# Performance work log

Measured on AMD Instinct MI355X. Metric: run time of the kernel, lower is better.

The kernel has to match this reference:

```python
import jax, jax.numpy as jnp
import numpy as np

H = 128
IN = 5
EPS = 1e-5


def lstm(x, Wih, Whh, bih, bhh):
    # x: [B,T,D]; PyTorch gate order i,f,g,o along 4H axis
    B, T, _ = x.shape
    xW = jnp.einsum('btd,gd->btg', x, Wih) + bih + bhh  # [B,T,4H]
    WhhT = Whh.T

    def step(carry, xt):
        h, c = carry
        g = xt + h @ WhhT
        i, f, gg, o = jnp.split(g, 4, axis=-1)
        i = jax.nn.sigmoid(i)
        f = jax.nn.sigmoid(f)
        gg = jnp.tanh(gg)
        o = jax.nn.sigmoid(o)
        c = f * c + i * gg
        h = o * jnp.tanh(c)
        return (h, c), h

    h0 = jnp.zeros((B, H), x.dtype)
    _, hs = jax.lax.scan(step, (h0, h0), jnp.swapaxes(xW, 0, 1))
    return jnp.swapaxes(hs, 0, 1)  # [B,T,H]


def batchnorm(x, gamma, beta):
    # training-mode BN over (batch, time) per channel; x: [B,T,H]
    mean = jnp.mean(x, axis=(0, 1))
    var = jnp.var(x, axis=(0, 1))
    return (x - mean) * (gamma * jax.lax.rsqrt(var + EPS)) + beta


def forward_one(x, Wih1, Whh1, bih1, bhh1, g1, b1, Wih2, Whh2, bih2, bhh2, g2, b2, fcW, fcb):
    out = lstm(x, Wih1, Whh1, bih1, bhh1)
    out = batchnorm(out, g1, b1)
    # dropout is identity (eval / deterministic reference)
    out = lstm(out, Wih2, Whh2, bih2, bhh2)
    out = batchnorm(out, g2, b2)
    emb = out[:, -1, :] @ fcW.T + fcb  # [B,128]
    norm = jnp.sqrt(jnp.sum(emb * emb, axis=1, keepdims=True))
    return emb / jnp.maximum(norm, 1e-12)  # F.normalize p=2


def setup_inputs() -> dict:
    key = jax.random.key(0)
    ks = jax.random.split(key, 20)
    B, T = 512, 128
    s_in = 1.0 / np.sqrt(H)
    d = {
        'a': jax.random.normal(ks[0], (B, T, IN), jnp.float32),
        'p': jax.random.normal(ks[1], (B, T, IN), jnp.float32),
        'n': jax.random.normal(ks[2], (B, T, IN), jnp.float32),
        'Wih1': jax.random.uniform(ks[3], (4 * H, IN), jnp.float32, -s_in, s_in),
        'Whh1': jax.random.uniform(ks[4], (4 * H, H), jnp.float32, -s_in, s_in),
        'bih1': jax.random.uniform(ks[5], (4 * H,), jnp.float32, -s_in, s_in),
        'bhh1': jax.random.uniform(ks[6], (4 * H,), jnp.float32, -s_in, s_in),
        'g1': jnp.ones((H,), jnp.float32),
        'b1': jnp.zeros((H,), jnp.float32),
        'Wih2': jax.random.uniform(ks[7], (4 * H, H), jnp.float32, -s_in, s_in),
        'Whh2': jax.random.uniform(ks[8], (4 * H, H), jnp.float32, -s_in, s_in),
        'bih2': jax.random.uniform(ks[9], (4 * H,), jnp.float32, -s_in, s_in),
        'bhh2': jax.random.uniform(ks[10], (4 * H,), jnp.float32, -s_in, s_in),
        'g2': jnp.ones((H,), jnp.float32),
        'b2': jnp.zeros((H,), jnp.float32),
        'fcW': jax.random.uniform(ks[11], (H, H), jnp.float32, -s_in, s_in),
        'fcb': jax.random.uniform(ks[12], (H,), jnp.float32, -s_in, s_in),
    }
    return d


def reference(a, p, n, Wih1, Whh1, bih1, bhh1, g1, b1, Wih2, Whh2, bih2, bhh2, g2, b2, fcW, fcb):
    f = lambda x: forward_one(x, Wih1, Whh1, bih1, bhh1, g1, b1, Wih2, Whh2, bih2, bhh2, g2, b2, fcW, fcb)
    return (f(a), f(p), f(n))
```

## Files before the change

kernel.cpp:

```cpp
#include <hip/hip_runtime.h>


typedef __attribute__((ext_vector_type(8))) _Float16 half8;
typedef __attribute__((ext_vector_type(4))) float f32x4;

#define TS 128
#define HID 128
#define NGATE 512
#define INV_N (1.0f/65536.0f)

#define BAR() asm volatile("s_waitcnt lgkmcnt(0)\n\ts_barrier" ::: "memory")

__device__ __forceinline__ float rcpf(float x) { return __builtin_amdgcn_rcpf(x); }
__device__ __forceinline__ float clamp20(float x) { return fminf(fmaxf(x, -20.0f), 20.0f); }

__device__ __forceinline__ _Float16 lstm_cell(float zi, float zf, float zg, float zo,
                                              float& c) {
  zg = clamp20(zg);
  float ei = __expf(-zi);
  float eg = __expf(-2.0f * zg);
  float ef = __expf(-zf);
  float fv = rcpf(1.0f + ef);
  float ig = (1.0f - eg) * rcpf((1.0f + ei) * (1.0f + eg));
  float cc = fv * c + ig;
  c = cc;
  float ccl = clamp20(cc);
  float eo = __expf(-zo);
  float ec = __expf(-2.0f * ccl);
  float hv = (1.0f - ec) * rcpf((1.0f + eo) * (1.0f + ec));
  return (_Float16)hv;
}


__global__ void prep_all(const float* __restrict__ xa, const float* __restrict__ xp,
                         const float* __restrict__ xn,
                         const float* __restrict__ Whh1, const float* __restrict__ Whh2,
                         const float* __restrict__ bih1, const float* __restrict__ bhh1,
                         _Float16* __restrict__ xpad,
                         _Float16* __restrict__ whhT1, _Float16* __restrict__ whhT2,
                         float* __restrict__ b1c) {
  int bid = blockIdx.x, tid = threadIdx.x;
  if (bid < 6144) {
    int i = bid * 256 + tid;
    int tile = i >> 14, rem = i & 16383;
    int t = rem >> 7, r = (rem >> 3) & 15, d = i & 7;
    int inp = tile >> 5, rloc = (tile & 31) * 16;
    const float* x = (inp == 0) ? xa : ((inp == 1) ? xp : xn);
    xpad[i] = (d < 5) ? (_Float16)x[(rloc + r) * 640 + t * 5 + d] : (_Float16)0.0f;
  } else if (bid < 6656) {
    int i = (bid - 6144) * 256 + tid;
    int which = i >> 16, idx = i & 65535;
    int k = idx >> 9, g = idx & 511;
    const float* src = which ? Whh2 : Whh1;
    (which ? whhT2 : whhT1)[idx] = (_Float16)src[g * HID + k];
  } else {
    int i = (bid - 6656) * 256 + tid;
    b1c[i] = bih1[i] + bhh1[i];
  }
}

__global__ __launch_bounds__(512, 2) void lstm1_kernel(
    const _Float16* __restrict__ xpad,
    const float* __restrict__ Wih1,
    const float* __restrict__ b1c,
    const _Float16* __restrict__ whhT,
    _Float16* __restrict__ hs1,
    float* __restrict__ s1sum, float* __restrict__ s1sq) {
  const int wg = blockIdx.x;
  const int inp = wg >> 5;
  const int tid = threadIdx.x;
  const int w = tid >> 6;
  const int lane = tid & 63;
  const int l15 = lane & 15;
  const int quad = lane >> 4;
  const int col = w * 16 + l15;
  const int kb = quad * 8;

  __shared__ _Float16 hb[2][2048];
  for (int i = tid; i < 4096; i += 512) ((_Float16*)hb)[i] = (_Float16)0.0f;

  const int rbase = (quad * 16 + l15) * 8;
  const int wbase = (w >> 1) * 512 + ((w & 1) * 2 + (l15 >> 3)) * 128 +
                    quad * 32 + (l15 & 7);

  half8 bh[4][4];
#pragma unroll
  for (int kt = 0; kt < 4; ++kt)
#pragma unroll
    for (int gt = 0; gt < 4; ++gt) {
      int gcol = gt * 128 + col;
      half8 v;
#pragma unroll
      for (int j = 0; j < 8; ++j) v[j] = whhT[(kt * 32 + kb + j) * NGATE + gcol];
      bh[kt][gt] = v;
    }
  half8 bx[4];
#pragma unroll
  for (int gt = 0; gt < 4; ++gt) {
    half8 v = {0, 0, 0, 0, 0, 0, 0, 0};
    if (quad == 0) {
#pragma unroll
      for (int j = 0; j < 5; ++j) v[j] = (_Float16)Wih1[(gt * 128 + col) * 5 + j];
    }
    bx[gt] = v;
  }
  f32x4 biasv[4];
#pragma unroll
  for (int gt = 0; gt < 4; ++gt) {
    float b = b1c[gt * 128 + col];
    biasv[gt][0] = b; biasv[gt][1] = b; biasv[gt][2] = b; biasv[gt][3] = b;
  }

  half8 xp = {0, 0, 0, 0, 0, 0, 0, 0};
  if (quad == 0) xp = *(const half8*)&xpad[((size_t)(wg * TS) * 16 + l15) * 8];

  float c[4] = {0, 0, 0, 0};
  float ssum = 0.0f, ssq = 0.0f;
  _Float16* hs1w = hs1 + (size_t)wg * TS * 2048;

  __syncthreads();

  for (int t = 0; t < TS; ++t) {
    f32x4 acc[4];
#pragma unroll
    for (int gt = 0; gt < 4; ++gt)
      acc[gt] = __builtin_amdgcn_mfma_f32_16x16x32_f16(xp, bx[gt], biasv[gt], 0, 0, 0);
    if (t + 1 < TS && quad == 0)
      xp = *(const half8*)&xpad[((size_t)(wg * TS + t + 1) * 16 + l15) * 8];
    BAR();
    if (t > 0) {
      float2 cp = *(const float2*)&hb[t & 1][tid * 4];
      *(float2*)&hs1w[(size_t)(t - 1) * 2048 + tid * 4] = cp;
    }
#pragma unroll
    for (int kt = 0; kt < 4; ++kt) {
      half8 ah = *(const half8*)&hb[t & 1][kt * 512 + rbase];
#pragma unroll
      for (int gt = 0; gt < 4; ++gt)
        acc[gt] = __builtin_amdgcn_mfma_f32_16x16x32_f16(ah, bh[kt][gt], acc[gt], 0, 0, 0);
    }
    const int wb = (t + 1) & 1;
#pragma unroll
    for (int r = 0; r < 4; ++r) {
      _Float16 hh = lstm_cell(acc[0][r], acc[1][r], acc[2][r], acc[3][r], c[r]);
      float hr = (float)hh;
      ssum += hr; ssq += hr * hr;
      hb[wb][wbase + r * 8] = hh;
    }
  }
  BAR();
  {
    float2 cp = *(const float2*)&hb[0][tid * 4];
    *(float2*)&hs1w[(size_t)(TS - 1) * 2048 + tid * 4] = cp;
  }
  float s = ssum, q = ssq;
  s += __shfl_xor(s, 16); s += __shfl_xor(s, 32);
  q += __shfl_xor(q, 16); q += __shfl_xor(q, 32);
  if (quad == 0) {
    atomicAdd(&s1sum[inp * HID + col], s);
    atomicAdd(&s1sq[inp * HID + col], q);
  }
}

__global__ void mid_kernel(const float* __restrict__ s1sum, const float* __restrict__ s1sq,
                           const float* __restrict__ g1, const float* __restrict__ b1,
                           const float* __restrict__ Wih2,
                           const float* __restrict__ bih2, const float* __restrict__ bhh2,
                           _Float16* __restrict__ w2s, float* __restrict__ bias2eff) {
  int bid = blockIdx.x, tid = threadIdx.x;
  if (bid < 768) {
    int i = bid * 256 + tid;
    int inp = i >> 16, rem = i & 65535, k = rem >> 9, g = rem & 511;
    float m = s1sum[inp * HID + k] * INV_N;
    float v = s1sq[inp * HID + k] * INV_N - m * m;
    float sc = g1[k] * rsqrtf(v + 1e-5f);
    w2s[i] = (_Float16)(sc * Wih2[g * HID + k]);
  } else {
    int i = (bid - 768) * 256 + tid;
    int inp = i >> 9, g = i & 511;
    float acc = bih2[g] + bhh2[g];
    for (int h = 0; h < HID; ++h) {
      float m = s1sum[inp * HID + h] * INV_N;
      float v = s1sq[inp * HID + h] * INV_N - m * m;
      float sc = g1[h] * rsqrtf(v + 1e-5f);
      acc += (b1[h] - m * sc) * Wih2[g * HID + h];
    }
    bias2eff[i] = acc;
  }
}

__global__ __launch_bounds__(512, 2) void lstm2_kernel(
    const _Float16* __restrict__ hs1,
    const _Float16* __restrict__ whhT2,
    const _Float16* __restrict__ w2s,
    const float* __restrict__ bias2eff,
    _Float16* __restrict__ h_last,
    float* __restrict__ s2sum, float* __restrict__ s2sq) {
  const int wg = blockIdx.x;
  const int inp = wg >> 5;
  const int gr0 = wg * 16;
  const int tid = threadIdx.x;
  const int w = tid >> 6;
  const int lane = tid & 63;
  const int l15 = lane & 15;
  const int quad = lane >> 4;
  const int col = w * 16 + l15;
  const int kb = quad * 8;

  __shared__ _Float16 hb[2][2048];
  for (int i = tid; i < 4096; i += 512) ((_Float16*)hb)[i] = (_Float16)0.0f;

  const int rbase = (quad * 16 + l15) * 8;
  const int wbase = (w >> 1) * 512 + ((w & 1) * 2 + (l15 >> 3)) * 128 +
                    quad * 32 + (l15 & 7);

  const _Float16* w2sI = w2s + (size_t)inp * HID * NGATE;
  half8 bh[4][4], bxw[4][4];
#pragma unroll
  for (int kt = 0; kt < 4; ++kt)
#pragma unroll
    for (int gt = 0; gt < 4; ++gt) {
      int gcol = gt * 128 + col;
      half8 vh, vx;
#pragma unroll
      for (int j = 0; j < 8; ++j) {
        vh[j] = whhT2[(kt * 32 + kb + j) * NGATE + gcol];
        vx[j] = w2sI[(kt * 32 + kb + j) * NGATE + gcol];
      }
      bh[kt][gt] = vh;
      bxw[kt][gt] = vx;
    }
  f32x4 biasv[4];
#pragma unroll
  for (int gt = 0; gt < 4; ++gt) {
    float b = bias2eff[inp * NGATE + gt * 128 + col];
    biasv[gt][0] = b; biasv[gt][1] = b; biasv[gt][2] = b; biasv[gt][3] = b;
  }

  const _Float16* hg = hs1 + (size_t)wg * TS * 2048;
  half8 a2A[4], a2B[4];
#pragma unroll
  for (int kt = 0; kt < 4; ++kt) {
    a2A[kt] = *(const half8*)&hg[kt * 512 + rbase];
    a2B[kt] = *(const half8*)&hg[(size_t)2048 + kt * 512 + rbase];
  }

  float c[4] = {0, 0, 0, 0};
  float ssum = 0.0f, ssq = 0.0f;

  __syncthreads();

  auto step = [&](int t, half8 (&cur)[4]) {
    f32x4 acc[4];
#pragma unroll
    for (int gt = 0; gt < 4; ++gt)
      acc[gt] = __builtin_amdgcn_mfma_f32_16x16x32_f16(cur[0], bxw[0][gt], biasv[gt], 0, 0, 0);
#pragma unroll
    for (int kt = 1; kt < 4; ++kt)
#pragma unroll
      for (int gt = 0; gt < 4; ++gt)
        acc[gt] = __builtin_amdgcn_mfma_f32_16x16x32_f16(cur[kt], bxw[kt][gt], acc[gt], 0, 0, 0);
    if (t + 2 < TS) {
#pragma unroll
      for (int kt = 0; kt < 4; ++kt)
        cur[kt] = *(const half8*)&hg[(size_t)(t + 2) * 2048 + kt * 512 + rbase];
    }
    BAR();
#pragma unroll
    for (int kt = 0; kt < 4; ++kt) {
      half8 ah = *(const half8*)&hb[t & 1][kt * 512 + rbase];
#pragma unroll
      for (int gt = 0; gt < 4; ++gt)
        acc[gt] = __builtin_amdgcn_mfma_f32_16x16x32_f16(ah, bh[kt][gt], acc[gt], 0, 0, 0);
    }
    const int wb = (t + 1) & 1;
#pragma unroll
    for (int r = 0; r < 4; ++r) {
      _Float16 hh = lstm_cell(acc[0][r], acc[1][r], acc[2][r], acc[3][r], c[r]);
      float hr = (float)hh;
      ssum += hr; ssq += hr * hr;
      hb[wb][wbase + r * 8] = hh;
      if (t == TS - 1) h_last[(size_t)(gr0 + quad * 4 + r) * HID + col] = hh;
    }
  };

  for (int t = 0; t < TS; t += 2) {
    step(t, a2A);
    step(t + 1, a2B);
  }

  float s = ssum, q = ssq;
  s += __shfl_xor(s, 16); s += __shfl_xor(s, 32);
  q += __shfl_xor(q, 16); q += __shfl_xor(q, 32);
  if (quad == 0) {
    atomicAdd(&s2sum[inp * HID + col], s);
    atomicAdd(&s2sq[inp * HID + col], q);
  }
}

__global__ __launch_bounds__(256, 1) void head_kernel(
    const _Float16* __restrict__ h_last,
    const float* __restrict__ s2sum, const float* __restrict__ s2sq,
    const float* __restrict__ g2, const float* __restrict__ b2,
    const float* __restrict__ fcW, const float* __restrict__ fcb,
    float* __restrict__ out) {
  const int wg = blockIdx.x;
  const int inp = wg >> 5;
  const int gr0 = wg * 16;
  const int tid = threadIdx.x;

  __shared__ float fcwT[128][132];
  __shared__ float bnh[16][132];
  __shared__ float s2[128], sh2[128];
  __shared__ float part[16][16];
  __shared__ float inv[16];

  if (tid < 128) {
    float m = s2sum[inp * HID + tid] * INV_N;
    float v = s2sq[inp * HID + tid] * INV_N - m * m;
    float s = g2[tid] * rsqrtf(v + 1e-5f);
    s2[tid] = s; sh2[tid] = b2[tid] - m * s;
  }
  for (int i = tid; i < 16384; i += 256) {
    int j = i >> 7, h = i & 127;
    fcwT[h][j] = fcW[i];
  }
  __syncthreads();
  {
    int row = tid >> 4, c0 = (tid & 15) * 8;
#pragma unroll
    for (int k = 0; k < 8; ++k) {
      int h = c0 + k;
      bnh[row][h] = (float)h_last[(gr0 + row) * HID + h] * s2[h] + sh2[h];
    }
  }
  __syncthreads();
  const int row = tid >> 4, jl = tid & 15;
  float emb[8];
  float sq = 0.0f;
#pragma unroll
  for (int jj = 0; jj < 8; ++jj) {
    int j = jl + jj * 16;
    float acc = fcb[j];
    for (int h = 0; h < HID; ++h) acc += bnh[row][h] * fcwT[h][j];
    emb[jj] = acc; sq += acc * acc;
  }
  part[row][jl] = sq;
  __syncthreads();
  if (tid < 16) {
    float s = 0.0f;
    for (int k = 0; k < 16; ++k) s += part[tid][k];
    float nrm = sqrtf(s);
    inv[tid] = 1.0f / fmaxf(nrm, 1e-12f);
  }
  __syncthreads();
#pragma unroll
  for (int jj = 0; jj < 8; ++jj)
    out[(gr0 + row) * HID + jl + jj * 16] = emb[jj] * inv[row];
}

extern "C" void kernel_launch(void* const* d_in, const int* in_sizes, int n_in,
                              void* d_out, int out_size, void* d_ws, size_t ws_size,
                              hipStream_t stream) {
  const float* a    = (const float*)d_in[0];
  const float* p    = (const float*)d_in[1];
  const float* nn   = (const float*)d_in[2];
  const float* Wih1 = (const float*)d_in[3];
  const float* Whh1 = (const float*)d_in[4];
  const float* bih1 = (const float*)d_in[5];
  const float* bhh1 = (const float*)d_in[6];
  const float* g1   = (const float*)d_in[7];
  const float* b1   = (const float*)d_in[8];
  const float* Wih2 = (const float*)d_in[9];
  const float* Whh2 = (const float*)d_in[10];
  const float* bih2 = (const float*)d_in[11];
  const float* bhh2 = (const float*)d_in[12];
  const float* g2   = (const float*)d_in[13];
  const float* b2   = (const float*)d_in[14];
  const float* fcW  = (const float*)d_in[15];
  const float* fcb  = (const float*)d_in[16];

  char* ws = (char*)d_ws;
  float* s1sum = (float*)(ws + 0);
  float* s1sq  = s1sum + 384;
  float* s2sum = s1sum + 768;
  float* s2sq  = s1sum + 1152;
  float* b1c      = (float*)(ws + 6144);
  float* bias2eff = (float*)(ws + 8192);
  _Float16* whhT1 = (_Float16*)(ws + 14336);
  _Float16* whhT2 = (_Float16*)(ws + 145408);
  _Float16* w2s   = (_Float16*)(ws + 276480);
  _Float16* hlast = (_Float16*)(ws + 669696);
  _Float16* xpad  = (_Float16*)(ws + 1062912);
  _Float16* hs1   = (_Float16*)(ws + 4208640);

  hipMemsetAsync(ws, 0, 6144, stream);

  prep_all<<<6658, 256, 0, stream>>>(a, p, nn, Whh1, Whh2, bih1, bhh1,
                                     xpad, whhT1, whhT2, b1c);
  lstm1_kernel<<<96, 512, 0, stream>>>(xpad, Wih1, b1c, whhT1, hs1, s1sum, s1sq);
  mid_kernel<<<774, 256, 0, stream>>>(s1sum, s1sq, g1, b1, Wih2, bih2, bhh2,
                                      w2s, bias2eff);
  lstm2_kernel<<<96, 512, 0, stream>>>(hs1, whhT2, w2s, bias2eff, hlast, s2sum, s2sq);
  head_kernel<<<96, 256, 0, stream>>>(hlast, s2sum, s2sq, g2, b2, fcW, fcb, (float*)d_out);
}
```

Measured before the change: 368.0 us.

## Fold exp2 scaling into weights, vectorize prep layouts, reorder recurrent step barriers

Pre-scales the gate weights and biases by -log2(e), or -2·log2(e) for the g gate, so the LSTM cell can use raw exp2 without multiplies, and clamps with fmed3. Weight layouts are changed so the recurrent kernels load half8 vectors directly instead of gathering scalars. The prep and mid kernels write 8 halves per thread and share BN scales through LDS, which cuts their grid sizes. In both recurrent loops the barrier moves to the top of each step with the LDS reads hoisted ahead of the MFMAs. BN statistics now come from fp32 h instead of the fp16-rounded value, and h_last is written once after the loop.

```diff
diff --git a/kernel.cpp b/kernel.cpp
--- a/kernel.cpp
+++ b/kernel.cpp
@@ -8,27 +8,33 @@
 #define HID 128
 #define NGATE 512
 #define INV_N (1.0f/65536.0f)
+#define NL2E  -1.4426950408889634f
+#define N2L2E -2.8853900817779268f
+#define GCLAMP 57.707801635558536f
 
 #define BAR() asm volatile("s_waitcnt lgkmcnt(0)\n\ts_barrier" ::: "memory")
 
 __device__ __forceinline__ float rcpf(float x) { return __builtin_amdgcn_rcpf(x); }
-__device__ __forceinline__ float clamp20(float x) { return fminf(fmaxf(x, -20.0f), 20.0f); }
-
-__device__ __forceinline__ _Float16 lstm_cell(float zi, float zf, float zg, float zo,
-                                              float& c) {
-  zg = clamp20(zg);
-  float ei = __expf(-zi);
-  float eg = __expf(-2.0f * zg);
-  float ef = __expf(-zf);
-  float fv = rcpf(1.0f + ef);
-  float ig = (1.0f - eg) * rcpf((1.0f + ei) * (1.0f + eg));
+__device__ __forceinline__ float ex2(float x) { return __builtin_amdgcn_exp2f(x); }
+
+__device__ __forceinline__ float lstm_cell(float zi, float zf, float zg, float zo,
+                                           float& c) {
+  float zgc = __builtin_amdgcn_fmed3f(zg, -GCLAMP, GCLAMP);
+  float ei = ex2(zi);
+  float ef = ex2(zf);
+  float eg = ex2(zgc);
+  float eo = ex2(zo);
+  float pi = 1.0f + ei, pg = 1.0f + eg, pf = 1.0f + ef;
+  float P = pi * pg;
+  float rd = rcpf(P * pf);
+  float fv = P * rd;
+  float ig = (1.0f - eg) * (pf * rd);
   float cc = fv * c + ig;
   c = cc;
-  float ccl = clamp20(cc);
-  float eo = __expf(-zo);
-  float ec = __expf(-2.0f * ccl);
+  float t2 = __builtin_amdgcn_fmed3f(cc * N2L2E, -GCLAMP, GCLAMP);
+  float ec = ex2(t2);
   float hv = (1.0f - ec) * rcpf((1.0f + eo) * (1.0f + ec));
-  return (_Float16)hv;
+  return hv;
 }
 
 
@@ -40,22 +46,32 @@
                          _Float16* __restrict__ whhT1, _Float16* __restrict__ whhT2,
                          float* __restrict__ b1c) {
   int bid = blockIdx.x, tid = threadIdx.x;
-  if (bid < 6144) {
+  if (bid < 768) {
     int i = bid * 256 + tid;
-    int tile = i >> 14, rem = i & 16383;
-    int t = rem >> 7, r = (rem >> 3) & 15, d = i & 7;
+    int tile = i >> 11, rem = i & 2047;
+    int t = rem >> 4, r = rem & 15;
     int inp = tile >> 5, rloc = (tile & 31) * 16;
     const float* x = (inp == 0) ? xa : ((inp == 1) ? xp : xn);
-    xpad[i] = (d < 5) ? (_Float16)x[(rloc + r) * 640 + t * 5 + d] : (_Float16)0.0f;
-  } else if (bid < 6656) {
-    int i = (bid - 6144) * 256 + tid;
-    int which = i >> 16, idx = i & 65535;
-    int k = idx >> 9, g = idx & 511;
+    const float* row = x + (size_t)(rloc + r) * 640 + t * 5;
+    half8 v = {0, 0, 0, 0, 0, 0, 0, 0};
+#pragma unroll
+    for (int j = 0; j < 5; ++j) v[j] = (_Float16)row[j];
+    *(half8*)&xpad[(size_t)i * 8] = v;
+  } else if (bid < 832) {
+    int i = (bid - 768) * 256 + tid;
+    int which = i >> 13, i8 = i & 8191;
+    int kq = i8 >> 9, g = i8 & 511;
+    int k0 = (kq >> 2) * 32 + (kq & 3) * 8;
+    float gs = ((g >> 7) == 2) ? N2L2E : NL2E;
     const float* src = which ? Whh2 : Whh1;
-    (which ? whhT2 : whhT1)[idx] = (_Float16)src[g * HID + k];
+    half8 v;
+#pragma unroll
+    for (int j = 0; j < 8; ++j) v[j] = (_Float16)(src[(size_t)g * HID + k0 + j] * gs);
+    *(half8*)&(which ? whhT2 : whhT1)[(size_t)i8 * 8] = v;
   } else {
-    int i = (bid - 6656) * 256 + tid;
-    b1c[i] = bih1[i] + bhh1[i];
+    int i = (bid - 832) * 256 + tid;
+    float gs = ((i >> 7) == 2) ? N2L2E : NL2E;
+    b1c[i] = (bih1[i] + bhh1[i]) * gs;
   }
 }
 
@@ -74,7 +90,6 @@
   const int l15 = lane & 15;
   const int quad = lane >> 4;
   const int col = w * 16 + l15;
-  const int kb = quad * 8;
 
   __shared__ _Float16 hb[2][2048];
   for (int i = tid; i < 4096; i += 512) ((_Float16*)hb)[i] = (_Float16)0.0f;
@@ -87,20 +102,17 @@
 #pragma unroll
   for (int kt = 0; kt < 4; ++kt)
 #pragma unroll
-    for (int gt = 0; gt < 4; ++gt) {
-      int gcol = gt * 128 + col;
-      half8 v;
-#pragma unroll
-      for (int j = 0; j < 8; ++j) v[j] = whhT[(kt * 32 + kb + j) * NGATE + gcol];
-      bh[kt][gt] = v;
-    }
+    for (int gt = 0; gt < 4; ++gt)
+      bh[kt][gt] = *(const half8*)&whhT[(size_t)((kt * 4 + quad) * 512 + gt * 128 + col) * 8];
+
   half8 bx[4];
 #pragma unroll
   for (int gt = 0; gt < 4; ++gt) {
     half8 v = {0, 0, 0, 0, 0, 0, 0, 0};
     if (quad == 0) {
-#pragma unroll
-      for (int j = 0; j < 5; ++j) v[j] = (_Float16)Wih1[(gt * 128 + col) * 5 + j];
+      float gs = (gt == 2) ? N2L2E : NL2E;
+#pragma unroll
+      for (int j = 0; j < 5; ++j) v[j] = (_Float16)(Wih1[(gt * 128 + col) * 5 + j] * gs);
     }
     bx[gt] = v;
   }
@@ -118,35 +130,37 @@
   float ssum = 0.0f, ssq = 0.0f;
   _Float16* hs1w = hs1 + (size_t)wg * TS * 2048;
 
-  __syncthreads();
-
   for (int t = 0; t < TS; ++t) {
+    BAR();
+    half8 ah[4];
+#pragma unroll
+    for (int kt = 0; kt < 4; ++kt)
+      ah[kt] = *(const half8*)&hb[t & 1][kt * 512 + rbase];
+    if (t > 0) {
+      float2 cp = *(const float2*)&hb[t & 1][tid * 4];
+      *(float2*)&hs1w[(size_t)(t - 1) * 2048 + tid * 4] = cp;
+    }
     f32x4 acc[4];
 #pragma unroll
     for (int gt = 0; gt < 4; ++gt)
       acc[gt] = __builtin_amdgcn_mfma_f32_16x16x32_f16(xp, bx[gt], biasv[gt], 0, 0, 0);
     if (t + 1 < TS && quad == 0)
       xp = *(const half8*)&xpad[((size_t)(wg * TS + t + 1) * 16 + l15) * 8];
-    BAR();
-    if (t > 0) {
-      float2 cp = *(const float2*)&hb[t & 1][tid * 4];
-      *(float2*)&hs1w[(size_t)(t - 1) * 2048 + tid * 4] = cp;
-    }
-#pragma unroll
-    for (int kt = 0; kt < 4; ++kt) {
-      half8 ah = *(const half8*)&hb[t & 1][kt * 512 + rbase];
+#pragma unroll
+    for (int kt = 0; kt < 4; ++kt)
 #pragma unroll
       for (int gt = 0; gt < 4; ++gt)
-        acc[gt] = __builtin_amdgcn_mfma_f32_16x16x32_f16(ah, bh[kt][gt], acc[gt], 0, 0, 0);
-    }
+        acc[gt] = __builtin_amdgcn_mfma_f32_16x16x32_f16(ah[kt], bh[kt][gt], acc[gt], 0, 0, 0);
     const int wb = (t + 1) & 1;
+    float hv4[4];
 #pragma unroll
     for (int r = 0; r < 4; ++r) {
-      _Float16 hh = lstm_cell(acc[0][r], acc[1][r], acc[2][r], acc[3][r], c[r]);
-      float hr = (float)hh;
-      ssum += hr; ssq += hr * hr;
-      hb[wb][wbase + r * 8] = hh;
-    }
+      float hv = lstm_cell(acc[0][r], acc[1][r], acc[2][r], acc[3][r], c[r]);
+      hb[wb][wbase + r * 8] = (_Float16)hv;
+      hv4[r] = hv;
+    }
+#pragma unroll
+    for (int r = 0; r < 4; ++r) { ssum += hv4[r]; ssq += hv4[r] * hv4[r]; }
   }
   BAR();
   {
@@ -168,24 +182,40 @@
                            const float* __restrict__ bih2, const float* __restrict__ bhh2,
                            _Float16* __restrict__ w2s, float* __restrict__ bias2eff) {
   int bid = blockIdx.x, tid = threadIdx.x;
-  if (bid < 768) {
+  __shared__ float scB[8];
+  __shared__ float shL[128];
+  if (bid < 96) {
     int i = bid * 256 + tid;
-    int inp = i >> 16, rem = i & 65535, k = rem >> 9, g = rem & 511;
-    float m = s1sum[inp * HID + k] * INV_N;
-    float v = s1sq[inp * HID + k] * INV_N - m * m;
-    float sc = g1[k] * rsqrtf(v + 1e-5f);
-    w2s[i] = (_Float16)(sc * Wih2[g * HID + k]);
+    int inp = i >> 13, i8 = i & 8191;
+    int kq = i8 >> 9, g = i8 & 511;
+    int k0 = (kq >> 2) * 32 + (kq & 3) * 8;
+    if (tid < 8) {
+      int k = k0 + tid;
+      float m = s1sum[inp * HID + k] * INV_N;
+      float v = s1sq[inp * HID + k] * INV_N - m * m;
+      scB[tid] = g1[k] * rsqrtf(v + 1e-5f);
+    }
+    __syncthreads();
+    float gs = ((g >> 7) == 2) ? N2L2E : NL2E;
+    const float* wr = Wih2 + (size_t)g * HID + k0;
+    half8 v;
+#pragma unroll
+    for (int j = 0; j < 8; ++j) v[j] = (_Float16)(scB[j] * wr[j] * gs);
+    *(half8*)&w2s[((size_t)inp * 8192 + i8) * 8] = v;
   } else {
-    int i = (bid - 768) * 256 + tid;
+    int i = (bid - 96) * 256 + tid;
     int inp = i >> 9, g = i & 511;
+    if (tid < 128) {
+      float m = s1sum[inp * HID + tid] * INV_N;
+      float v = s1sq[inp * HID + tid] * INV_N - m * m;
+      float s = g1[tid] * rsqrtf(v + 1e-5f);
+      shL[tid] = b1[tid] - m * s;
+    }
+    __syncthreads();
     float acc = bih2[g] + bhh2[g];
-    for (int h = 0; h < HID; ++h) {
-      float m = s1sum[inp * HID + h] * INV_N;
-      float v = s1sq[inp * HID + h] * INV_N - m * m;
-      float sc = g1[h] * rsqrtf(v + 1e-5f);
-      acc += (b1[h] - m * sc) * Wih2[g * HID + h];
-    }
-    bias2eff[i] = acc;
+    for (int h = 0; h < HID; ++h) acc += shL[h] * Wih2[(size_t)g * HID + h];
+    float gs = ((g >> 7) == 2) ? N2L2E : NL2E;
+    bias2eff[i] = acc * gs;
   }
 }
 
@@ -205,7 +235,6 @@
   const int l15 = lane & 15;
   const int quad = lane >> 4;
   const int col = w * 16 + l15;
-  const int kb = quad * 8;
 
   __shared__ _Float16 hb[2][2048];
   for (int i = tid; i < 4096; i += 512) ((_Float16*)hb)[i] = (_Float16)0.0f;
@@ -220,15 +249,9 @@
   for (int kt = 0; kt < 4; ++kt)
 #pragma unroll
     for (int gt = 0; gt < 4; ++gt) {
-      int gcol = gt * 128 + col;
-      half8 vh, vx;
-#pragma unroll
-      for (int j = 0; j < 8; ++j) {
-        vh[j] = whhT2[(kt * 32 + kb + j) * NGATE + gcol];
-        vx[j] = w2sI[(kt * 32 + kb + j) * NGATE + gcol];
-      }
-      bh[kt][gt] = vh;
-      bxw[kt][gt] = vx;
+      size_t gi = (size_t)((kt * 4 + quad) * 512 + gt * 128 + col) * 8;
+      bh[kt][gt] = *(const half8*)&whhT2[gi];
+      bxw[kt][gt] = *(const half8*)&w2sI[gi];
     }
   f32x4 biasv[4];
 #pragma unroll
@@ -248,9 +271,12 @@
   float c[4] = {0, 0, 0, 0};
   float ssum = 0.0f, ssq = 0.0f;
 
-  __syncthreads();
-
   auto step = [&](int t, half8 (&cur)[4]) {
+    BAR();
+    half8 ah[4];
+#pragma unroll
+    for (int kt = 0; kt < 4; ++kt)
+      ah[kt] = *(const half8*)&hb[t & 1][kt * 512 + rbase];
     f32x4 acc[4];
 #pragma unroll
     for (int gt = 0; gt < 4; ++gt)
@@ -265,29 +291,32 @@
       for (int kt = 0; kt < 4; ++kt)
         cur[kt] = *(const half8*)&hg[(size_t)(t + 2) * 2048 + kt * 512 + rbase];
     }
-    BAR();
-#pragma unroll
-    for (int kt = 0; kt < 4; ++kt) {
-      half8 ah = *(const half8*)&hb[t & 1][kt * 512 + rbase];
+#pragma unroll
+    for (int kt = 0; kt < 4; ++kt)
 #pragma unroll
       for (int gt = 0; gt < 4; ++gt)
-        acc[gt] = __builtin_amdgcn_mfma_f32_16x16x32_f16(ah, bh[kt][gt], acc[gt], 0, 0, 0);
-    }
+        acc[gt] = __builtin_amdgcn_mfma_f32_16x16x32_f16(ah[kt], bh[kt][gt], acc[gt], 0, 0, 0);
     const int wb = (t + 1) & 1;
+    float hv4[4];
 #pragma unroll
     for (int r = 0; r < 4; ++r) {
-      _Float16 hh = lstm_cell(acc[0][r], acc[1][r], acc[2][r], acc[3][r], c[r]);
-      float hr = (float)hh;
-      ssum += hr; ssq += hr * hr;
-      hb[wb][wbase + r * 8] = hh;
-      if (t == TS - 1) h_last[(size_t)(gr0 + quad * 4 + r) * HID + col] = hh;
-    }
+      float hv = lstm_cell(acc[0][r], acc[1][r], acc[2][r], acc[3][r], c[r]);
+      hb[wb][wbase + r * 8] = (_Float16)hv;
+      hv4[r] = hv;
+    }
+#pragma unroll
+    for (int r = 0; r < 4; ++r) { ssum += hv4[r]; ssq += hv4[r] * hv4[r]; }
   };
 
   for (int t = 0; t < TS; t += 2) {
     step(t, a2A);
     step(t + 1, a2B);
   }
+
+  BAR();
+#pragma unroll
+  for (int r = 0; r < 4; ++r)
+    h_last[(size_t)(gr0 + quad * 4 + r) * HID + col] = hb[0][wbase + r * 8];
 
   float s = ssum, q = ssq;
   s += __shfl_xor(s, 16); s += __shfl_xor(s, 32);
@@ -396,10 +425,10 @@
 
   hipMemsetAsync(ws, 0, 6144, stream);
 
-  prep_all<<<6658, 256, 0, stream>>>(a, p, nn, Whh1, Whh2, bih1, bhh1,
-                                     xpad, whhT1, whhT2, b1c);
+  prep_all<<<834, 256, 0, stream>>>(a, p, nn, Whh1, Whh2, bih1, bhh1,
+                                    xpad, whhT1, whhT2, b1c);
   lstm1_kernel<<<96, 512, 0, stream>>>(xpad, Wih1, b1c, whhT1, hs1, s1sum, s1sq);
-  mid_kernel<<<774, 256, 0, stream>>>(s1sum, s1sq, g1, b1, Wih2, bih2, bhh2,
+  mid_kernel<<<102, 256, 0, stream>>>(s1sum, s1sq, g1, b1, Wih2, bih2, bhh2,
                                       w2s, bias2eff);
   lstm2_kernel<<<96, 512, 0, stream>>>(hs1, whhT2, w2s, bias2eff, hlast, s2sum, s2sq);
   head_kernel<<<96, 256, 0, stream>>>(hlast, s2sum, s2sq, g2, b2, fcW, fcb, (float*)d_out);
```

After: 337.1 us. 1.09x faster.
